# Performance work log

Hardware: AMD Instinct MI355X
Metric: run time of the kernel (lower is better)

Reference implementation:

```python
import jax, jax.numpy as jnp
import numpy as np
from jax import lax

B, T, D, H, O, L = 32, 2048, 256, 256, 256, 2


def setup_inputs() -> dict:
    key = jax.random.key(0)
    ks = jax.random.split(key, 16)
    s = 0.05
    inp = {"x": jax.random.normal(ks[0], (B, T, D), dtype=jnp.float32)}
    dims = [D, H]  # input dim of each layer
    for l in range(L):
        inp[f"Wi{l}"] = jax.random.normal(ks[1 + 3 * l], (dims[l], 4 * H), dtype=jnp.float32) * s
        inp[f"Wh{l}"] = jax.random.normal(ks[2 + 3 * l], (H, 4 * H), dtype=jnp.float32) * s
        inp[f"b{l}"] = jnp.zeros((4 * H,), dtype=jnp.float32)
    inp["Wd"] = jax.random.normal(ks[10], (H, O), dtype=jnp.float32) * s
    inp["bd"] = jnp.zeros((O,), dtype=jnp.float32)
    return inp


def _lstm_layer(x, Wi, Wh, b):
    # x: [B, T, Din] -> outputs h over time: [B, T, H]
    Bx = x.shape[0]
    Hh = Wh.shape[0]
    # Precompute input projections for all timesteps (one big GEMM).
    xg = jnp.einsum('btd,dg->tbg', x, Wi)  # time-major [T, B, 4H]

    def step(carry, xg_t):
        c, h = carry
        z = xg_t + h @ Wh + b  # [B, 4H]
        i, f, g, o = jnp.split(z, 4, axis=-1)  # flax gate order: i, f, g, o
        c_new = jax.nn.sigmoid(f) * c + jax.nn.sigmoid(i) * jnp.tanh(g)
        h_new = jax.nn.sigmoid(o) * jnp.tanh(c_new)
        return (c_new, h_new), h_new

    c0 = jnp.zeros((Bx, Hh), dtype=x.dtype)
    h0 = jnp.zeros((Bx, Hh), dtype=x.dtype)
    _, ys = lax.scan(step, (c0, h0), xg)  # ys: [T, B, H]
    return ys.transpose(1, 0, 2)


def reference(x, Wi0, Wh0, b0, Wi1, Wh1, b1, Wd, bd):
    y = _lstm_layer(x, Wi0, Wh0, b0)
    y = _lstm_layer(y, Wi1, Wh1, b1)
    last_hidden = y[:, -1]  # [B, H]
    return last_hidden @ Wd + bd  # [B, O]
```

## Files before the change

kernel.cpp:

```cpp
#include <hip/hip_runtime.h>
#include <stdint.h>

#define TT 2048
#define DD 256
#define GG 1024
#define HWORDS 8192
#define RING0 64
#define RING1 4
#define PROW 1024

typedef __attribute__((ext_vector_type(4))) float f32x4;
typedef __attribute__((ext_vector_type(8))) short s16x8;
typedef __attribute__((ext_vector_type(4))) unsigned u32x4;

static __device__ __forceinline__ unsigned f2bf(float f) {
    union { float f; unsigned u; } v; v.f = f;
    return (v.u + 0x7fffu + ((v.u >> 16) & 1u)) >> 16;
}
static __device__ __forceinline__ float bf2f(unsigned b) {
    union { unsigned u; float f; } v; v.u = b << 16;
    return v.f;
}
static __device__ __forceinline__ float sigm(float x) {
    return 1.0f / (1.0f + __expf(-x));
}
static __device__ __forceinline__ float tanh_f(float x) {
    x = fminf(15.0f, fmaxf(-15.0f, x));
    float e = __expf(2.0f * x);
    return (e - 1.0f) / (e + 1.0f);
}

static __device__ __forceinline__ u32x4 ld16_sys(const unsigned* p) {
    u32x4 r;
    asm volatile("global_load_dwordx4 %0, %1, off sc0 sc1"
                 : "=&v"(r) : "v"(p) : "memory");
    return r;
}
static __device__ __forceinline__ u32x4 ld16(const unsigned* p) {
    u32x4 r;
    asm volatile("global_load_dwordx4 %0, %1, off"
                 : "=&v"(r) : "v"(p) : "memory");
    return r;
}
static __device__ __forceinline__ void st4_sys(unsigned* p, unsigned d) {
    asm volatile("global_store_dword %0, %1, off sc0 sc1" :: "v"(p), "v"(d) : "memory");
}

#define VW(n) do { asm volatile("s_waitcnt vmcnt(" #n ")" ::: "memory"); \
                   __builtin_amdgcn_sched_barrier(0); } while (0)
#define LBAR() do { asm volatile("s_waitcnt lgkmcnt(0)\n\ts_barrier" ::: "memory"); \
                    __builtin_amdgcn_sched_barrier(0); } while (0)

static __device__ __forceinline__ bool tags_ok4(const u32x4 v[8], unsigned tag) {
    unsigned d = 0;
#pragma unroll
    for (int i = 0; i < 8; ++i)
        d |= (v[i][0] ^ tag) | (v[i][1] ^ tag) | (v[i][2] ^ tag) | (v[i][3] ^ tag);
    return (d & 0xffffu) == 0;
}

__global__ void k_init(unsigned* __restrict__ h0, unsigned* __restrict__ h1) {
    unsigned i = blockIdx.x * 256 + threadIdx.x;
    h0[i] = 0u;
    if (i < RING1 * HWORDS) h1[i] = 0u;
}

__launch_bounds__(256, 1)
__global__ void k_scan(const float* __restrict__ x,
                       const float* __restrict__ Wi0, const float* __restrict__ Wh0,
                       const float* __restrict__ b0,
                       const float* __restrict__ Wi1, const float* __restrict__ Wh1,
                       const float* __restrict__ b1,
                       unsigned* h0w, unsigned* h1w)
{
    const int tid = threadIdx.x;
    const bool isL0 = (blockIdx.x < 32);
    const int w = blockIdx.x & 31;

    const float* Wi = isL0 ? Wi0 : Wi1;
    const float* Wh = isL0 ? Wh0 : Wh1;
    const float* bb = isL0 ? b0 : b1;

    __shared__ __align__(16) unsigned char Ap[32 * PROW];
    __shared__ float zbuf[4 * 32 * 10];

    const int lane = tid & 63;
    const int wid = tid >> 6;
    const int mt = wid & 1;
    const int nt = wid >> 1;

    s16x8 Bf[16];
    {
        const int jloc = lane & 15;
        const int lcol = nt * 16 + jloc;
        const int gate = lcol >> 3;
        const int jj = lcol & 7;
        const int gcol = gate * 256 + w * 8 + jj;
        const int krow = (lane >> 4) * 8;
#pragma unroll
        for (int kf = 0; kf < 16; ++kf) {
            s16x8 a;
#pragma unroll
            for (int j = 0; j < 8; ++j) {
                int k = kf * 32 + krow + j;
                float wv = (k < 256) ? Wi[(size_t)k * GG + gcol] : Wh[(size_t)(k - 256) * GG + gcol];
                a[j] = (short)f2bf(wv);
            }
            Bf[kf] = a;
        }
    }

    const int gm = tid >> 3;
    const int gj = tid & 7;
    const float bi_ = bb[0 * 256 + w * 8 + gj], bf_ = bb[1 * 256 + w * 8 + gj];
    const float bg_ = bb[2 * 256 + w * 8 + gj], bo_ = bb[3 * 256 + w * 8 + gj];

    const int cb = tid & 63;
    const int rq = tid >> 6;
    const int hword = gm * 256 + w * 8 + gj;

    const unsigned arow = (unsigned)(mt * 16 + (lane & 15));
    const unsigned rb = arow * PROW;
    const unsigned asw = (arow & 7u) << 4;

    float cs = 0.f;
    long long budget = 500000;

    if (isL0) {
        int known = 0;
        u32x4 xr[8];
#pragma unroll
        for (int i = 0; i < 8; ++i)
            xr[i] = ld16((const unsigned*)(x + (size_t)(i * 4 + rq) * (TT * DD) + cb * 4));
        VW(0);

        for (int c = 0; c < TT; ++c) {
#pragma unroll
            for (int i = 0; i < 8; ++i) {
                unsigned row = (unsigned)(i * 4 + rq);
                uint2 pk;
                pk.x = f2bf(__uint_as_float(xr[i][0])) | (f2bf(__uint_as_float(xr[i][1])) << 16);
                pk.y = f2bf(__uint_as_float(xr[i][2])) | (f2bf(__uint_as_float(xr[i][3])) << 16);
                *(uint2*)(Ap + row * PROW + (((unsigned)(cb * 8)) ^ ((row & 7u) << 4))) = pk;
            }
            const unsigned* s0 = h0w + (size_t)(c & (RING0 - 1)) * HWORDS + tid * 4;
            u32x4 pv[8];
#pragma unroll
            for (int i = 0; i < 8; ++i) pv[i] = ld16_sys(s0 + i * 1024);
            if (c + 1 < TT) {
#pragma unroll
                for (int i = 0; i < 8; ++i)
                    xr[i] = ld16((const unsigned*)(x + (size_t)(i * 4 + rq) * (TT * DD)
                                                   + (size_t)(c + 1) * DD + cb * 4));
            }
            LBAR();

            f32x4 acc = {0.f, 0.f, 0.f, 0.f};
#pragma unroll
            for (int kf = 0; kf < 8; ++kf) {
                unsigned kb = (unsigned)kf * 64u + ((unsigned)(lane >> 4)) * 16u;
                s16x8 a = *(const s16x8*)(Ap + rb + (kb ^ asw));
                acc = __builtin_amdgcn_mfma_f32_16x16x32_bf16(a, Bf[kf], acc, 0, 0, 0);
            }
            if (c + 1 < TT) VW(8); else VW(0);
            while (!tags_ok4(pv, (unsigned)c)) {
                if (--budget <= 0) break;
                __builtin_amdgcn_s_sleep(1);
#pragma unroll
                for (int i = 0; i < 8; ++i) pv[i] = ld16_sys(s0 + i * 1024);
                VW(0);
            }
#pragma unroll
            for (int i = 0; i < 8; ++i) {
                unsigned row = (unsigned)(i * 4 + rq);
                uint2 pk;
                pk.x = (pv[i][0] >> 16) | (pv[i][1] & 0xffff0000u);
                pk.y = (pv[i][2] >> 16) | (pv[i][3] & 0xffff0000u);
                *(uint2*)(Ap + row * PROW + ((512u + (unsigned)cb * 8u) ^ ((row & 7u) << 4))) = pk;
            }
            LBAR();

#pragma unroll
            for (int kf = 8; kf < 16; ++kf) {
                unsigned kb = (unsigned)kf * 64u + ((unsigned)(lane >> 4)) * 16u;
                s16x8 a = *(const s16x8*)(Ap + rb + (kb ^ asw));
                acc = __builtin_amdgcn_mfma_f32_16x16x32_bf16(a, Bf[kf], acc, 0, 0, 0);
            }
            {
                const int n = nt * 16 + (lane & 15);
                const int g = n >> 3, cl = n & 7;
#pragma unroll
                for (int r = 0; r < 4; ++r)
                    zbuf[g * 320 + (mt * 16 + (lane >> 4) * 4 + r) * 10 + cl] = acc[r];
            }
            VW(0);
            LBAR();

            float zi = zbuf[0 * 320 + gm * 10 + gj] + bi_;
            float zf = zbuf[1 * 320 + gm * 10 + gj] + bf_;
            float zg = zbuf[2 * 320 + gm * 10 + gj] + bg_;
            float zo = zbuf[3 * 320 + gm * 10 + gj] + bo_;
            cs = sigm(zf) * cs + sigm(zi) * tanh_f(zg);
            float h = sigm(zo) * tanh_f(cs);

            int T = c - 63;
            if (T > known) {
                const unsigned* trow = h1w + (size_t)(T & (RING1 - 1)) * HWORDS + lane * 4;
                for (;;) {
                    u32x4 tv = ld16_sys(trow);
                    VW(0);
                    int m = (int)(tv[0] & 0xffffu);
                    m = min(m, (int)(tv[1] & 0xffffu));
                    m = min(m, (int)(tv[2] & 0xffffu));
                    m = min(m, (int)(tv[3] & 0xffffu));
#pragma unroll
                    for (int off = 32; off; off >>= 1) m = min(m, __shfl_xor(m, off, 64));
                    if (m >= T) { known = m; break; }
                    if (--budget <= 0) break;
                    __builtin_amdgcn_s_sleep(4);
                }
            }
            st4_sys(h0w + (size_t)((c + 1) & (RING0 - 1)) * HWORDS + hword,
                    (f2bf(h) << 16) | (unsigned)(c + 1));
        }
    } else {
        u32x4 ph[8];
        {
            const unsigned* sp = h0w + (size_t)(1 & (RING0 - 1)) * HWORDS + tid * 4;
#pragma unroll
            for (int i = 0; i < 8; ++i) ph[i] = ld16_sys(sp + i * 1024);
        }
        for (int c = 0; c < TT; ++c) {
            const unsigned* s0 = h0w + (size_t)((c + 1) & (RING0 - 1)) * HWORDS + tid * 4;
            if (c == 0) VW(0); else VW(1);
            while (!tags_ok4(ph, (unsigned)(c + 1))) {
                if (--budget <= 0) break;
                __builtin_amdgcn_s_sleep(1);
#pragma unroll
                for (int i = 0; i < 8; ++i) ph[i] = ld16_sys(s0 + i * 1024);
                VW(0);
            }
#pragma unroll
            for (int i = 0; i < 8; ++i) {
                unsigned row = (unsigned)(i * 4 + rq);
                uint2 pk;
                pk.x = (ph[i][0] >> 16) | (ph[i][1] & 0xffff0000u);
                pk.y = (ph[i][2] >> 16) | (ph[i][3] & 0xffff0000u);
                *(uint2*)(Ap + row * PROW + (((unsigned)(cb * 8)) ^ ((row & 7u) << 4))) = pk;
            }
            const unsigned* s1 = h1w + (size_t)(c & (RING1 - 1)) * HWORDS + tid * 4;
            u32x4 qv[8];
#pragma unroll
            for (int i = 0; i < 8; ++i) qv[i] = ld16_sys(s1 + i * 1024);
            LBAR();

            f32x4 acc = {0.f, 0.f, 0.f, 0.f};
#pragma unroll
            for (int kf = 0; kf < 8; ++kf) {
                unsigned kb = (unsigned)kf * 64u + ((unsigned)(lane >> 4)) * 16u;
                s16x8 a = *(const s16x8*)(Ap + rb + (kb ^ asw));
                acc = __builtin_amdgcn_mfma_f32_16x16x32_bf16(a, Bf[kf], acc, 0, 0, 0);
            }
            VW(0);
            while (!tags_ok4(qv, (unsigned)c)) {
                if (--budget <= 0) break;
                __builtin_amdgcn_s_sleep(1);
#pragma unroll
                for (int i = 0; i < 8; ++i) qv[i] = ld16_sys(s1 + i * 1024);
                VW(0);
            }
#pragma unroll
            for (int i = 0; i < 8; ++i) {
                unsigned row = (unsigned)(i * 4 + rq);
                uint2 pk;
                pk.x = (qv[i][0] >> 16) | (qv[i][1] & 0xffff0000u);
                pk.y = (qv[i][2] >> 16) | (qv[i][3] & 0xffff0000u);
                *(uint2*)(Ap + row * PROW + ((512u + (unsigned)cb * 8u) ^ ((row & 7u) << 4))) = pk;
            }
            LBAR();

#pragma unroll
            for (int kf = 8; kf < 16; ++kf) {
                unsigned kb = (unsigned)kf * 64u + ((unsigned)(lane >> 4)) * 16u;
                s16x8 a = *(const s16x8*)(Ap + rb + (kb ^ asw));
                acc = __builtin_amdgcn_mfma_f32_16x16x32_bf16(a, Bf[kf], acc, 0, 0, 0);
            }
            {
                const int n = nt * 16 + (lane & 15);
                const int g = n >> 3, cl = n & 7;
#pragma unroll
                for (int r = 0; r < 4; ++r)
                    zbuf[g * 320 + (mt * 16 + (lane >> 4) * 4 + r) * 10 + cl] = acc[r];
            }
            LBAR();

            float zi = zbuf[0 * 320 + gm * 10 + gj] + bi_;
            float zf = zbuf[1 * 320 + gm * 10 + gj] + bf_;
            float zg = zbuf[2 * 320 + gm * 10 + gj] + bg_;
            float zo = zbuf[3 * 320 + gm * 10 + gj] + bo_;
            cs = sigm(zf) * cs + sigm(zi) * tanh_f(zg);
            float h = sigm(zo) * tanh_f(cs);

            if (c + 1 < TT) {
                const unsigned* sn = h0w + (size_t)((c + 2) & (RING0 - 1)) * HWORDS + tid * 4;
#pragma unroll
                for (int i = 0; i < 8; ++i) ph[i] = ld16_sys(sn + i * 1024);
            }
            st4_sys(h1w + (size_t)((c + 1) & (RING1 - 1)) * HWORDS + hword,
                    (f2bf(h) << 16) | (unsigned)(c + 1));
        }
    }
}

__global__ void k_dense(const unsigned* __restrict__ h1last,
                        const float* __restrict__ Wd, const float* __restrict__ bd,
                        float* __restrict__ out)
{
    __shared__ float hs[256];
    const int m = blockIdx.x;
    const int o = threadIdx.x;
    hs[o] = bf2f(h1last[m * 256 + o] >> 16);
    __syncthreads();
    float acc = bd[o];
#pragma unroll 8
    for (int k = 0; k < 256; ++k)
        acc = fmaf(hs[k], Wd[k * 256 + o], acc);
    out[m * 256 + o] = acc;
}

extern "C" void kernel_launch(void* const* d_in, const int* in_sizes, int n_in,
                              void* d_out, int out_size, void* d_ws, size_t ws_size,
                              hipStream_t stream)
{
    const float* x   = (const float*)d_in[0];
    const float* Wi0 = (const float*)d_in[1];
    const float* Wh0 = (const float*)d_in[2];
    const float* b0  = (const float*)d_in[3];
    const float* Wi1 = (const float*)d_in[4];
    const float* Wh1 = (const float*)d_in[5];
    const float* b1  = (const float*)d_in[6];
    const float* Wd  = (const float*)d_in[7];
    const float* bd  = (const float*)d_in[8];
    float* out = (float*)d_out;

    char* ws = (char*)d_ws;
    unsigned* h0w = (unsigned*)ws;
    unsigned* h1w = (unsigned*)(ws + (size_t)RING0 * HWORDS * 4);

    k_init<<<dim3(RING0 * HWORDS / 256), dim3(256), 0, stream>>>(h0w, h1w);
    k_scan<<<dim3(64), dim3(256), 0, stream>>>(x, Wi0, Wh0, b0, Wi1, Wh1, b1, h0w, h1w);
    k_dense<<<dim3(32), dim3(256), 0, stream>>>(
        h1w + (size_t)(TT & (RING1 - 1)) * HWORDS, Wd, bd, out);
}
```

Before: 4.939 ms.

## Double-buffer hidden-state polling and reorder the ring layout into per-block contiguous stores

The spin-wait on the hidden-state ring now keeps two in-flight load sets (A/B), issuing a second poll right after the first MFMA half so a ready value is found sooner without a full round trip. The ring layout is changed so each block writes a contiguous 256-word slice (w*256+tid), and the unpack/LDS scatter and dense-kernel read are adjusted to match. The x prefetch for the next step is moved after the poll and a redundant VW(0) is dropped. This adds register pressure and more complex polling logic, and the layout remap must stay consistent across producers and consumers.

```diff
diff --git a/kernel.cpp b/kernel.cpp
--- a/kernel.cpp
+++ b/kernel.cpp
@@ -50,6 +50,9 @@
                    __builtin_amdgcn_sched_barrier(0); } while (0)
 #define LBAR() do { asm volatile("s_waitcnt lgkmcnt(0)\n\ts_barrier" ::: "memory"); \
                     __builtin_amdgcn_sched_barrier(0); } while (0)
+
+#define KEEP8(a) asm volatile("" :: "v"(a[0]), "v"(a[1]), "v"(a[2]), "v"(a[3]), \
+                                    "v"(a[4]), "v"(a[5]), "v"(a[6]), "v"(a[7]))
 
 static __device__ __forceinline__ bool tags_ok4(const u32x4 v[8], unsigned tag) {
     unsigned d = 0;
@@ -117,7 +120,9 @@
 
     const int cb = tid & 63;
     const int rq = tid >> 6;
-    const int hword = gm * 256 + w * 8 + gj;
+
+    const unsigned urow = (unsigned)((tid >> 1) & 31);
+    const unsigned usw = (urow & 7u) << 4;
 
     const unsigned arow = (unsigned)(mt * 16 + (lane & 15));
     const unsigned rb = arow * PROW;
@@ -126,6 +131,15 @@
     float cs = 0.f;
     long long budget = 500000;
 
+#define UNP_STORE(A0, A1, A2, A3, BASE, I) do {                                   \
+        uint2 pk_;                                                                \
+        pk_.x = ((A0) >> 16) | ((A1) & 0xffff0000u);                              \
+        pk_.y = ((A2) >> 16) | ((A3) & 0xffff0000u);                              \
+        unsigned bcol_ = (unsigned)((I) * 4 + (tid >> 6)) * 16u                   \
+                       + (unsigned)(tid & 1) * 8u;                                \
+        *(uint2*)(Ap + urow * PROW + (((BASE) + bcol_) ^ usw)) = pk_;             \
+    } while (0)
+
     if (isL0) {
         int known = 0;
         u32x4 xr[8];
@@ -133,8 +147,11 @@
         for (int i = 0; i < 8; ++i)
             xr[i] = ld16((const unsigned*)(x + (size_t)(i * 4 + rq) * (TT * DD) + cb * 4));
         VW(0);
+        u32x4 pA[8] = {}, pB[8] = {};
 
         for (int c = 0; c < TT; ++c) {
+            VW(1);
+            KEEP8(pA); KEEP8(pB);
 #pragma unroll
             for (int i = 0; i < 8; ++i) {
                 unsigned row = (unsigned)(i * 4 + rq);
@@ -144,15 +161,8 @@
                 *(uint2*)(Ap + row * PROW + (((unsigned)(cb * 8)) ^ ((row & 7u) << 4))) = pk;
             }
             const unsigned* s0 = h0w + (size_t)(c & (RING0 - 1)) * HWORDS + tid * 4;
-            u32x4 pv[8];
-#pragma unroll
-            for (int i = 0; i < 8; ++i) pv[i] = ld16_sys(s0 + i * 1024);
-            if (c + 1 < TT) {
-#pragma unroll
-                for (int i = 0; i < 8; ++i)
-                    xr[i] = ld16((const unsigned*)(x + (size_t)(i * 4 + rq) * (TT * DD)
-                                                   + (size_t)(c + 1) * DD + cb * 4));
-            }
+#pragma unroll
+            for (int i = 0; i < 8; ++i) pA[i] = ld16_sys(s0 + i * 1024);
             LBAR();
 
             f32x4 acc = {0.f, 0.f, 0.f, 0.f};
@@ -162,21 +172,39 @@
                 s16x8 a = *(const s16x8*)(Ap + rb + (kb ^ asw));
                 acc = __builtin_amdgcn_mfma_f32_16x16x32_bf16(a, Bf[kf], acc, 0, 0, 0);
             }
-            if (c + 1 < TT) VW(8); else VW(0);
-            while (!tags_ok4(pv, (unsigned)c)) {
-                if (--budget <= 0) break;
-                __builtin_amdgcn_s_sleep(1);
-#pragma unroll
-                for (int i = 0; i < 8; ++i) pv[i] = ld16_sys(s0 + i * 1024);
-                VW(0);
+#pragma unroll
+            for (int i = 0; i < 8; ++i) pB[i] = ld16_sys(s0 + i * 1024);
+            VW(8);
+            bool wA = tags_ok4(pA, (unsigned)c);
+            bool ok = wA;
+            while (!ok) {
+                if (--budget <= 0) break;
+                __builtin_amdgcn_s_sleep(1);
+#pragma unroll
+                for (int i = 0; i < 8; ++i) pA[i] = ld16_sys(s0 + i * 1024);
+                VW(8);
+                if (tags_ok4(pB, (unsigned)c)) { ok = true; wA = false; break; }
+                if (--budget <= 0) break;
+                __builtin_amdgcn_s_sleep(1);
+#pragma unroll
+                for (int i = 0; i < 8; ++i) pB[i] = ld16_sys(s0 + i * 1024);
+                VW(8);
+                wA = tags_ok4(pA, (unsigned)c);
+                ok = wA;
             }
 #pragma unroll
             for (int i = 0; i < 8; ++i) {
-                unsigned row = (unsigned)(i * 4 + rq);
-                uint2 pk;
-                pk.x = (pv[i][0] >> 16) | (pv[i][1] & 0xffff0000u);
-                pk.y = (pv[i][2] >> 16) | (pv[i][3] & 0xffff0000u);
-                *(uint2*)(Ap + row * PROW + ((512u + (unsigned)cb * 8u) ^ ((row & 7u) << 4))) = pk;
+                unsigned a0 = wA ? pA[i][0] : pB[i][0];
+                unsigned a1 = wA ? pA[i][1] : pB[i][1];
+                unsigned a2 = wA ? pA[i][2] : pB[i][2];
+                unsigned a3 = wA ? pA[i][3] : pB[i][3];
+                UNP_STORE(a0, a1, a2, a3, 512u, i);
+            }
+            if (c + 1 < TT) {
+#pragma unroll
+                for (int i = 0; i < 8; ++i)
+                    xr[i] = ld16((const unsigned*)(x + (size_t)(i * 4 + rq) * (TT * DD)
+                                                   + (size_t)(c + 1) * DD + cb * 4));
             }
             LBAR();
 
@@ -193,7 +221,6 @@
                 for (int r = 0; r < 4; ++r)
                     zbuf[g * 320 + (mt * 16 + (lane >> 4) * 4 + r) * 10 + cl] = acc[r];
             }
-            VW(0);
             LBAR();
 
             float zi = zbuf[0 * 320 + gm * 10 + gj] + bi_;
@@ -205,7 +232,8 @@
 
             int T = c - 63;
             if (T > known) {
-                const unsigned* trow = h1w + (size_t)(T & (RING1 - 1)) * HWORDS + lane * 4;
+                const unsigned* trow = h1w + (size_t)(T & (RING1 - 1)) * HWORDS
+                                     + (size_t)(lane & 31) * 256;
                 for (;;) {
                     u32x4 tv = ld16_sys(trow);
                     VW(0);
@@ -220,19 +248,20 @@
                     __builtin_amdgcn_s_sleep(4);
                 }
             }
-            st4_sys(h0w + (size_t)((c + 1) & (RING0 - 1)) * HWORDS + hword,
+            st4_sys(h0w + (size_t)((c + 1) & (RING0 - 1)) * HWORDS + w * 256 + tid,
                     (f2bf(h) << 16) | (unsigned)(c + 1));
         }
     } else {
-        u32x4 ph[8];
+        u32x4 ph[8], qA[8] = {}, qB[8] = {};
         {
-            const unsigned* sp = h0w + (size_t)(1 & (RING0 - 1)) * HWORDS + tid * 4;
+            const unsigned* sp = h0w + (size_t)1 * HWORDS + tid * 4;
 #pragma unroll
             for (int i = 0; i < 8; ++i) ph[i] = ld16_sys(sp + i * 1024);
         }
         for (int c = 0; c < TT; ++c) {
+            if (c == 0) { VW(0); } else { VW(1); }
+            KEEP8(qA); KEEP8(qB);
             const unsigned* s0 = h0w + (size_t)((c + 1) & (RING0 - 1)) * HWORDS + tid * 4;
-            if (c == 0) VW(0); else VW(1);
             while (!tags_ok4(ph, (unsigned)(c + 1))) {
                 if (--budget <= 0) break;
                 __builtin_amdgcn_s_sleep(1);
@@ -241,17 +270,12 @@
                 VW(0);
             }
 #pragma unroll
-            for (int i = 0; i < 8; ++i) {
-                unsigned row = (unsigned)(i * 4 + rq);
-                uint2 pk;
-                pk.x = (ph[i][0] >> 16) | (ph[i][1] & 0xffff0000u);
-                pk.y = (ph[i][2] >> 16) | (ph[i][3] & 0xffff0000u);
-                *(uint2*)(Ap + row * PROW + (((unsigned)(cb * 8)) ^ ((row & 7u) << 4))) = pk;
-            }
+            for (int i = 0; i < 8; ++i)
+                UNP_STORE(ph[i][0], ph[i][1], ph[i][2], ph[i][3], 0u, i);
+
             const unsigned* s1 = h1w + (size_t)(c & (RING1 - 1)) * HWORDS + tid * 4;
-            u32x4 qv[8];
-#pragma unroll
-            for (int i = 0; i < 8; ++i) qv[i] = ld16_sys(s1 + i * 1024);
+#pragma unroll
+            for (int i = 0; i < 8; ++i) qA[i] = ld16_sys(s1 + i * 1024);
             LBAR();
 
             f32x4 acc = {0.f, 0.f, 0.f, 0.f};
@@ -261,21 +285,33 @@
                 s16x8 a = *(const s16x8*)(Ap + rb + (kb ^ asw));
                 acc = __builtin_amdgcn_mfma_f32_16x16x32_bf16(a, Bf[kf], acc, 0, 0, 0);
             }
-            VW(0);
-            while (!tags_ok4(qv, (unsigned)c)) {
-                if (--budget <= 0) break;
-                __builtin_amdgcn_s_sleep(1);
-#pragma unroll
-                for (int i = 0; i < 8; ++i) qv[i] = ld16_sys(s1 + i * 1024);
-                VW(0);
+#pragma unroll
+            for (int i = 0; i < 8; ++i) qB[i] = ld16_sys(s1 + i * 1024);
+            VW(8);
+            bool wA = tags_ok4(qA, (unsigned)c);
+            bool ok = wA;
+            while (!ok) {
+                if (--budget <= 0) break;
+                __builtin_amdgcn_s_sleep(1);
+#pragma unroll
+                for (int i = 0; i < 8; ++i) qA[i] = ld16_sys(s1 + i * 1024);
+                VW(8);
+                if (tags_ok4(qB, (unsigned)c)) { ok = true; wA = false; break; }
+                if (--budget <= 0) break;
+                __builtin_amdgcn_s_sleep(1);
+#pragma unroll
+                for (int i = 0; i < 8; ++i) qB[i] = ld16_sys(s1 + i * 1024);
+                VW(8);
+                wA = tags_ok4(qA, (unsigned)c);
+                ok = wA;
             }
 #pragma unroll
             for (int i = 0; i < 8; ++i) {
-                unsigned row = (unsigned)(i * 4 + rq);
-                uint2 pk;
-                pk.x = (qv[i][0] >> 16) | (qv[i][1] & 0xffff0000u);
-                pk.y = (qv[i][2] >> 16) | (qv[i][3] & 0xffff0000u);
-                *(uint2*)(Ap + row * PROW + ((512u + (unsigned)cb * 8u) ^ ((row & 7u) << 4))) = pk;
+                unsigned a0 = wA ? qA[i][0] : qB[i][0];
+                unsigned a1 = wA ? qA[i][1] : qB[i][1];
+                unsigned a2 = wA ? qA[i][2] : qB[i][2];
+                unsigned a3 = wA ? qA[i][3] : qB[i][3];
+                UNP_STORE(a0, a1, a2, a3, 512u, i);
             }
             LBAR();
 
@@ -306,10 +342,11 @@
 #pragma unroll
                 for (int i = 0; i < 8; ++i) ph[i] = ld16_sys(sn + i * 1024);
             }
-            st4_sys(h1w + (size_t)((c + 1) & (RING1 - 1)) * HWORDS + hword,
+            st4_sys(h1w + (size_t)((c + 1) & (RING1 - 1)) * HWORDS + w * 256 + tid,
                     (f2bf(h) << 16) | (unsigned)(c + 1));
         }
     }
+#undef UNP_STORE
 }
 
 __global__ void k_dense(const unsigned* __restrict__ h1last,
@@ -319,7 +356,7 @@
     __shared__ float hs[256];
     const int m = blockIdx.x;
     const int o = threadIdx.x;
-    hs[o] = bf2f(h1last[m * 256 + o] >> 16);
+    hs[o] = bf2f(h1last[(o >> 3) * 256 + m * 8 + (o & 7)] >> 16);
     __syncthreads();
     float acc = bd[o];
 #pragma unroll 8
```

Result: faster. 4.634 ms (-6.2%).
